# Optimization experiments

Measured on AMD Instinct MI355X. Metric: run time of the kernel, lower is better.

## Reference

```python
import jax, jax.numpy as jnp
import numpy as np

DIM = 8
EPS = 1e-6
TRIL = DIM * (DIM + 1) // 2  # 36


def _build_L(params):
    # params: [N, TRIL] -> lower-triangular L: [N, DIM, DIM] with diag clamped >= 1e-4
    rows, cols = jnp.tril_indices(DIM)
    L = jnp.zeros((params.shape[0], DIM, DIM), params.dtype)
    L = L.at[:, rows, cols].set(params)
    idx = jnp.arange(DIM)
    d = jnp.clip(L[:, idx, idx], 0.0001)
    return L.at[:, idx, idx].set(d)


def _compute_density(L):
    # L: [N, DIM, DIM] -> PSD trace-1 density matrices [N, DIM, DIM]
    I = jnp.eye(DIM, dtype=L.dtype)
    rho = jnp.einsum('nij,nkj->nik', L, L) + EPS * I
    w = jnp.linalg.eigvalsh(rho)                      # [N, DIM]
    corr = jnp.maximum(-w.min(axis=-1), 0.0) + 1e-6   # shift to PSD
    rho = rho + corr[:, None, None] * I
    tr = jnp.trace(rho, axis1=1, axis2=2)
    return rho / (tr[:, None, None] + EPS)


def _matrix_sqrt(x):
    U, S, Vh = jnp.linalg.svd(x, full_matrices=False)
    sqrt_S = jnp.sqrt(S + EPS)
    return (U * sqrt_S[..., None, :]) @ Vh


def _quantum_fidelity(rho, sigma):
    sqrt_rho = _matrix_sqrt(rho)
    product = sqrt_rho @ sigma @ sqrt_rho
    S = jnp.linalg.svd(product, compute_uv=False)
    f = jnp.sum(jnp.sqrt(S + EPS), axis=-1)
    return jnp.clip(f, 0.0, 1.0)


def setup_inputs() -> dict:
    key = jax.random.key(0)
    k1, k2, k3 = jax.random.split(key, 3)
    B, S, V = 16384, 10, 100000
    contexts = jax.random.randint(k1, (B, S), 0, V)
    targets = jax.random.randint(k2, (B,), 0, V)
    # embedding table, init roughly like the torch module (uniform + diag ramp)
    emb_weight = jax.random.uniform(k3, (V, TRIL), jnp.float32, -0.1, 0.1)
    diag_idx = np.array([i * (i + 1) // 2 + i for i in range(DIM)])
    diag_vals = jnp.linspace(0.1, 1.0, DIM, dtype=jnp.float32)
    emb_weight = emb_weight.at[:, diag_idx].set(jnp.broadcast_to(diag_vals, (V, DIM)))
    return {"contexts": contexts, "targets": targets, "emb_weight": emb_weight}


def reference(contexts, targets, emb_weight):
    B, S = contexts.shape
    # context density matrices
    ctx_params = jnp.take(emb_weight, contexts.reshape(-1), axis=0)   # [B*S, TRIL]
    rho_ctx = _compute_density(_build_L(ctx_params)).reshape(B, S, DIM, DIM)
    mask = (contexts != 0).astype(rho_ctx.dtype)[:, :, None, None]
    context_rho = (rho_ctx * mask).sum(axis=1) / mask.sum(axis=1)     # [B, DIM, DIM]
    # target density matrices
    tgt_params = jnp.take(emb_weight, targets, axis=0)                # [B, TRIL]
    rho_tgt = _compute_density(_build_L(tgt_params))                  # [B, DIM, DIM]
    f = _quantum_fidelity(context_rho, rho_tgt)                       # [B]
    return -jnp.log(jnp.clip(f, 1e-8))
```

## Files before the change

### kernel.cpp

```cpp
#include <hip/hip_runtime.h>
#include <math.h>

#define NB   16384
#define SEQ  10
#define DIM  8
#define TRIL 36

__device__ __forceinline__ constexpr int tri(int r, int c) { return r * (r + 1) / 2 + c; }

template <int CTRL>
__device__ __forceinline__ float fperm(float v) {
    return __int_as_float(__builtin_amdgcn_mov_dpp(__float_as_int(v), CTRL, 0xf, 0xf, true));
}
template <int CTRL>
__device__ __forceinline__ double dperm(double v) {
    long long u = __double_as_longlong(v);
    int lo = (int)(u & 0xffffffffLL);
    int hi = (int)(u >> 32);
    lo = __builtin_amdgcn_mov_dpp(lo, CTRL, 0xf, 0xf, true);
    hi = __builtin_amdgcn_mov_dpp(hi, CTRL, 0xf, 0xf, true);
    return __longlong_as_double(((long long)hi << 32) | (long long)(unsigned)lo);
}

__device__ __forceinline__ double fast_rsqrt(double x) {
    double r = __builtin_amdgcn_rsq(x);
    r = r * (1.5 - 0.5 * x * r * r);
    r = r * (1.5 - 0.5 * x * r * r);
    return r;
}
__device__ __forceinline__ double fast_rcp(double x) {
    double r = __builtin_amdgcn_rcp(x);
    r = r * (2.0 - x * r);
    r = r * (2.0 - x * r);
    return r;
}
__device__ __forceinline__ double fast_sqrt(double x) { return x * fast_rsqrt(x); }

template <bool ACCUM>
__device__ __forceinline__ void add_density(const float* __restrict__ p, double (&dst)[TRIL]) {
    float Lf[TRIL];
    const float4* p4 = (const float4*)p;
    #pragma unroll
    for (int i = 0; i < 9; ++i) {
        float4 v = p4[i];
        Lf[4*i+0] = v.x; Lf[4*i+1] = v.y; Lf[4*i+2] = v.z; Lf[4*i+3] = v.w;
    }
    #pragma unroll
    for (int d = 0; d < DIM; ++d) Lf[tri(d, d)] = fmaxf(Lf[tri(d, d)], 1.0e-4f);

    double tr = 1.6e-5;
    #pragma unroll
    for (int i = 0; i < TRIL; ++i) { double v = (double)Lf[i]; tr += v * v; }
    double inv = fast_rcp(tr + 1.0e-6);

    #pragma unroll
    for (int i = 0; i < DIM; ++i) {
        #pragma unroll
        for (int j = 0; j <= i; ++j) {
            double sum = (i == j) ? 2.0e-6 : 0.0;
            #pragma unroll
            for (int k = 0; k <= j; ++k) sum += (double)Lf[tri(i, k)] * (double)Lf[tri(j, k)];
            if (ACCUM) dst[tri(i, j)] += sum * inv;
            else       dst[tri(i, j)]  = sum * inv;
        }
    }
}

__device__ __forceinline__ void chol36(double (&M)[TRIL]) {
    #pragma unroll
    for (int j = 0; j < DIM; ++j) {
        double d = M[tri(j, j)];
        #pragma unroll
        for (int k = 0; k < j; ++k) d -= M[tri(j, k)] * M[tri(j, k)];
        d = fmax(d, 1.0e-30);
        double invd = fast_rsqrt(d);
        M[tri(j, j)] = d * invd;
        #pragma unroll
        for (int i = j + 1; i < DIM; ++i) {
            double v = M[tri(i, j)];
            #pragma unroll
            for (int k = 0; k < j; ++k) v -= M[tri(i, k)] * M[tri(j, k)];
            M[tri(i, j)] = v * invd;
        }
    }
}

__global__ void __launch_bounds__(64)
qcbow_kernel(const int* __restrict__ contexts,
             const int* __restrict__ targets,
             const float* __restrict__ emb,
             float* __restrict__ out)
{
    const int tid = blockIdx.x * 64 + threadIdx.x;
    const int b = tid >> 2;
    const int g = threadIdx.x & 3;

    double A[TRIL];
    #pragma unroll
    for (int i = 0; i < TRIL; ++i) A[i] = 0.0;
    float cntf = 0.0f;
    for (int s = g; s < SEQ; s += 4) {
        int tok = contexts[b * SEQ + s];
        if (tok != 0) {
            add_density<true>(emb + (size_t)tok * TRIL, A);
            cntf += 1.0f;
        }
    }

    double W[TRIL];
    add_density<false>(emb + (size_t)targets[b] * TRIL, W);

    #pragma unroll
    for (int i = 0; i < TRIL; ++i) A[i] += dperm<0xB1>(A[i]);
    cntf += fperm<0xB1>(cntf);
    #pragma unroll
    for (int i = 0; i < TRIL; ++i) A[i] += dperm<0x4E>(A[i]);
    cntf += fperm<0x4E>(cntf);

    chol36(W);

    double invc = fast_rcp((double)cntf);
    #pragma unroll
    for (int i = 0; i < TRIL; ++i) A[i] *= invc;
    #pragma unroll
    for (int d = 0; d < DIM; ++d) A[tri(d, d)] += 1.0e-6;
    chol36(A);

    double wa[DIM], wb[DIM];
#define PICKW(JA, JB)                                                              \
    {                                                                              \
        _Pragma("unroll")                                                          \
        for (int k = 0; k < DIM; ++k) wa[k] = (k >= (JA)) ? W[tri(k, (JA))] : 0.0; \
        _Pragma("unroll")                                                          \
        for (int k = 0; k < DIM; ++k) wb[k] = (k >= (JB)) ? W[tri(k, (JB))] : 0.0; \
    }
    switch (g) {
        case 0: PICKW(0, 1); break;
        case 1: PICKW(2, 3); break;
        case 2: PICKW(4, 5); break;
        default: PICKW(6, 7); break;
    }
#undef PICKW

    float a[DIM], bb[DIM];
    #pragma unroll
    for (int i = 0; i < DIM; ++i) {
        double sa = 0.0, sb = 0.0;
        #pragma unroll
        for (int k = i; k < DIM; ++k) {
            double lk = A[tri(k, i)];
            sa += lk * wa[k];
            sb += lk * wb[k];
        }
        a[i] = (float)sa; bb[i] = (float)sb;
    }

    for (int sweep = 0; sweep < 8; ++sweep) {
        bool conv = true;
        #pragma unroll
        for (int r = 0; r < 7; ++r) {
            float x = 0.0f, y = 0.0f, z = 0.0f;
            #pragma unroll
            for (int k = 0; k < DIM; ++k) {
                x = fmaf(a[k], a[k], x);
                y = fmaf(bb[k], bb[k], y);
                z = fmaf(a[k], bb[k], z);
            }
            float z2 = z * z;
            float d  = x - y;
            if (z2 > 1.0e-12f * x * y && z2 > 1.0e-12f * d * d) conv = false;
            if (z2 > 1.0e-16f * x * y) {
                float tau = -d * (0.5f * __builtin_amdgcn_rcpf(z));
                float t = __builtin_amdgcn_rcpf(fabsf(tau) + sqrtf(fmaf(tau, tau, 1.0f)));
                t = (tau >= 0.0f) ? t : -t;
                float c = __builtin_amdgcn_rsqf(fmaf(t, t, 1.0f));
                float s = t * c;
                #pragma unroll
                for (int k = 0; k < DIM; ++k) {
                    float na = c * a[k] - s * bb[k];
                    float nb = s * a[k] + c * bb[k];
                    a[k] = na; bb[k] = nb;
                }
            }
            #pragma unroll
            for (int k = 0; k < DIM; ++k) {
                float olda = a[k];
                float sa = (g == 0) ? bb[k] : a[k];
                float ta = fperm<0x93>(sa);
                float tb = fperm<0x39>(bb[k]);
                a[k]  = (g == 0) ? olda : ta;
                bb[k] = (g == 3) ? olda : tb;
            }
        }
        if (sweep >= 2 && __all(conv)) break;
    }

    double xn = 0.0, yn = 0.0;
    #pragma unroll
    for (int k = 0; k < DIM; ++k) {
        xn += (double)a[k] * (double)a[k];
        yn += (double)bb[k] * (double)bb[k];
    }
    double fp = fast_sqrt(xn + 1.0e-6) + fast_sqrt(yn + 1.0e-6);
    fp += dperm<0xB1>(fp);
    fp += dperm<0x4E>(fp);
    if (g == 0) {
        double f = fmin(fp, 1.0);
        f = fmax(f, 1.0e-8);
        out[b] = (float)(-log(f));
    }
}

extern "C" void kernel_launch(void* const* d_in, const int* in_sizes, int n_in,
                              void* d_out, int out_size, void* d_ws, size_t ws_size,
                              hipStream_t stream) {
    const int*   contexts = (const int*)d_in[0];
    const int*   targets  = (const int*)d_in[1];
    const float* emb      = (const float*)d_in[2];
    float*       out      = (float*)d_out;

    qcbow_kernel<<<dim3(NB * 4 / 64), dim3(64), 0, stream>>>(contexts, targets, emb, out);
}
```

Measured before the change: 85.81 us.

## Spread each batch item over eight lanes with one-column-per-lane Jacobi

Each batch element is now handled by 8 lanes instead of 4. Every lane loads its context and target rows up front, and the two Cholesky factorizations (context and target) run in parallel on separate half-groups. The result is exchanged with ds_swizzle. The one-sided Jacobi SVD is reorganised so each lane owns one column, using a round-robin partner exchange through DPP and swizzle. This cuts per-thread serial work and register pressure, at the cost of more cross-lane shuffles and duplicated density computation for the target on some lanes.

New measurement: 86.99 us. About the same (+1.4%).

```diff
diff --git a/kernel.cpp b/kernel.cpp
--- a/kernel.cpp
+++ b/kernel.cpp
@@ -16,9 +16,20 @@
 __device__ __forceinline__ double dperm(double v) {
     long long u = __double_as_longlong(v);
     int lo = (int)(u & 0xffffffffLL);
-    int hi = (int)(u >> 32);
+    int hi = (int)(((unsigned long long)u) >> 32);
     lo = __builtin_amdgcn_mov_dpp(lo, CTRL, 0xf, 0xf, true);
     hi = __builtin_amdgcn_mov_dpp(hi, CTRL, 0xf, 0xf, true);
+    return __longlong_as_double(((long long)hi << 32) | (long long)(unsigned)lo);
+}
+__device__ __forceinline__ float fswz4(float v) {
+    return __int_as_float(__builtin_amdgcn_ds_swizzle(__float_as_int(v), 0x101F));
+}
+__device__ __forceinline__ double dswz4(double v) {
+    long long u = __double_as_longlong(v);
+    int lo = (int)(u & 0xffffffffLL);
+    int hi = (int)(((unsigned long long)u) >> 32);
+    lo = __builtin_amdgcn_ds_swizzle(lo, 0x101F);
+    hi = __builtin_amdgcn_ds_swizzle(hi, 0x101F);
     return __longlong_as_double(((long long)hi << 32) | (long long)(unsigned)lo);
 }
 
@@ -36,23 +47,23 @@
 }
 __device__ __forceinline__ double fast_sqrt(double x) { return x * fast_rsqrt(x); }
 
+__device__ __forceinline__ void load_row(const float* __restrict__ emb, int tok, float (&F)[TRIL]) {
+    const float4* q = (const float4*)(emb + (size_t)tok * TRIL);
+    #pragma unroll
+    for (int i = 0; i < 9; ++i) {
+        float4 v = q[i];
+        F[4*i+0] = v.x; F[4*i+1] = v.y; F[4*i+2] = v.z; F[4*i+3] = v.w;
+    }
+}
+
 template <bool ACCUM>
-__device__ __forceinline__ void add_density(const float* __restrict__ p, double (&dst)[TRIL]) {
-    float Lf[TRIL];
-    const float4* p4 = (const float4*)p;
-    #pragma unroll
-    for (int i = 0; i < 9; ++i) {
-        float4 v = p4[i];
-        Lf[4*i+0] = v.x; Lf[4*i+1] = v.y; Lf[4*i+2] = v.z; Lf[4*i+3] = v.w;
-    }
+__device__ __forceinline__ void density_from(float (&Lf)[TRIL], double (&dst)[TRIL]) {
     #pragma unroll
     for (int d = 0; d < DIM; ++d) Lf[tri(d, d)] = fmaxf(Lf[tri(d, d)], 1.0e-4f);
-
     double tr = 1.6e-5;
     #pragma unroll
     for (int i = 0; i < TRIL; ++i) { double v = (double)Lf[i]; tr += v * v; }
     double inv = fast_rcp(tr + 1.0e-6);
-
     #pragma unroll
     for (int i = 0; i < DIM; ++i) {
         #pragma unroll
@@ -85,30 +96,72 @@
     }
 }
 
-__global__ void __launch_bounds__(64)
+template <int M>
+__device__ __forceinline__ float jrecv(float v) {
+    if constexpr (M == 1) return fperm<0xB1>(v);
+    else if constexpr (M == 2) return fperm<0x4E>(v);
+    else if constexpr (M == 3) return fperm<0x1B>(v);
+    else return __int_as_float(__builtin_amdgcn_ds_swizzle(__float_as_int(v), (M << 10) | 0x1F));
+}
+template <int M>
+__device__ __forceinline__ void jround(float (&o)[DIM], bool& conv) {
+    float r[DIM];
+    #pragma unroll
+    for (int k = 0; k < DIM; ++k) r[k] = jrecv<M>(o[k]);
+    float xo = 0.0f, xr = 0.0f, z = 0.0f;
+    #pragma unroll
+    for (int k = 0; k < DIM; ++k) {
+        xo = fmaf(o[k], o[k], xo);
+        xr = fmaf(r[k], r[k], xr);
+        z  = fmaf(o[k], r[k], z);
+    }
+    float z2 = z * z;
+    float d  = xr - xo;
+    if (z2 > 1.0e-12f * xo * xr && z2 > 1.0e-12f * d * d) conv = false;
+    if (z2 > 1.0e-16f * xo * xr) {
+        float tau = d * (0.5f * __builtin_amdgcn_rcpf(z));
+        float t = __builtin_amdgcn_rcpf(fabsf(tau) + sqrtf(fmaf(tau, tau, 1.0f)));
+        t = (tau >= 0.0f) ? t : -t;
+        float c = __builtin_amdgcn_rsqf(fmaf(t, t, 1.0f));
+        float s = t * c;
+        #pragma unroll
+        for (int k = 0; k < DIM; ++k) o[k] = fmaf(c, o[k], -s * r[k]);
+    }
+}
+
+__global__ void __launch_bounds__(256, 2)
 qcbow_kernel(const int* __restrict__ contexts,
              const int* __restrict__ targets,
              const float* __restrict__ emb,
              float* __restrict__ out)
 {
-    const int tid = blockIdx.x * 64 + threadIdx.x;
-    const int b = tid >> 2;
-    const int g = threadIdx.x & 3;
+    const int tid = blockIdx.x * 256 + threadIdx.x;
+    const int b = tid >> 3;
+    const int h = threadIdx.x & 7;
+
+    const int base = b * SEQ;
+    int tok1 = contexts[base + h];
+    int tok2 = 0;
+    if (h < 2)  tok2 = contexts[base + 8 + h];
+    if (h >= 4) tok2 = targets[b];
+
+    float F1[TRIL], F2[TRIL];
+    load_row(emb, tok1, F1);
+    load_row(emb, tok2, F2);
 
     double A[TRIL];
     #pragma unroll
     for (int i = 0; i < TRIL; ++i) A[i] = 0.0;
     float cntf = 0.0f;
-    for (int s = g; s < SEQ; s += 4) {
-        int tok = contexts[b * SEQ + s];
-        if (tok != 0) {
-            add_density<true>(emb + (size_t)tok * TRIL, A);
-            cntf += 1.0f;
-        }
-    }
-
-    double W[TRIL];
-    add_density<false>(emb + (size_t)targets[b] * TRIL, W);
+
+    if (tok1 != 0) { density_from<true>(F1, A); cntf = 1.0f; }
+    double T[TRIL];
+    density_from<false>(F2, T);
+    if (h < 2 && tok2 != 0) {
+        #pragma unroll
+        for (int i = 0; i < TRIL; ++i) A[i] += T[i];
+        cntf += 1.0f;
+    }
 
     #pragma unroll
     for (int i = 0; i < TRIL; ++i) A[i] += dperm<0xB1>(A[i]);
@@ -116,95 +169,76 @@
     #pragma unroll
     for (int i = 0; i < TRIL; ++i) A[i] += dperm<0x4E>(A[i]);
     cntf += fperm<0x4E>(cntf);
-
-    chol36(W);
+    #pragma unroll
+    for (int i = 0; i < TRIL; ++i) A[i] += dswz4(A[i]);
+    cntf += fswz4(cntf);
 
     double invc = fast_rcp((double)cntf);
     #pragma unroll
     for (int i = 0; i < TRIL; ++i) A[i] *= invc;
     #pragma unroll
     for (int d = 0; d < DIM; ++d) A[tri(d, d)] += 1.0e-6;
-    chol36(A);
-
-    double wa[DIM], wb[DIM];
-#define PICKW(JA, JB)                                                              \
-    {                                                                              \
-        _Pragma("unroll")                                                          \
-        for (int k = 0; k < DIM; ++k) wa[k] = (k >= (JA)) ? W[tri(k, (JA))] : 0.0; \
-        _Pragma("unroll")                                                          \
-        for (int k = 0; k < DIM; ++k) wb[k] = (k >= (JB)) ? W[tri(k, (JB))] : 0.0; \
-    }
-    switch (g) {
-        case 0: PICKW(0, 1); break;
-        case 1: PICKW(2, 3); break;
-        case 2: PICKW(4, 5); break;
-        default: PICKW(6, 7); break;
-    }
-#undef PICKW
-
-    float a[DIM], bb[DIM];
+
+    const bool q0 = (h < 4);
+    double M[TRIL];
+    #pragma unroll
+    for (int i = 0; i < TRIL; ++i) M[i] = q0 ? A[i] : T[i];
+    chol36(M);
+
+    double Rm[TRIL];
+    #pragma unroll
+    for (int i = 0; i < TRIL; ++i) Rm[i] = dswz4(M[i]);
+
+    double Lw_[TRIL];
+    #pragma unroll
+    for (int i = 0; i < TRIL; ++i) Lw_[i] = q0 ? Rm[i] : M[i];
+    const bool h1 = (h & 1), h2 = (h & 2), h4 = (h & 4);
+    double w[DIM];
+    #pragma unroll
+    for (int k = 0; k < DIM; ++k) {
+        #define E(J) ((k >= (J)) ? Lw_[tri((k >= (J)) ? k : (J), (J))] : 0.0)
+        double m0 = h1 ? E(1) : E(0);
+        double m1 = h1 ? E(3) : E(2);
+        double m2 = h1 ? E(5) : E(4);
+        double m3 = h1 ? E(7) : E(6);
+        #undef E
+        double n0 = h2 ? m1 : m0;
+        double n1 = h2 ? m3 : m2;
+        w[k] = h4 ? n1 : n0;
+    }
+
+    float col[DIM];
     #pragma unroll
     for (int i = 0; i < DIM; ++i) {
-        double sa = 0.0, sb = 0.0;
+        double s = 0.0;
         #pragma unroll
         for (int k = i; k < DIM; ++k) {
-            double lk = A[tri(k, i)];
-            sa += lk * wa[k];
-            sb += lk * wb[k];
+            double lc = q0 ? M[tri(k, i)] : Rm[tri(k, i)];
+            s += lc * w[k];
         }
-        a[i] = (float)sa; bb[i] = (float)sb;
+        col[i] = (float)s;
     }
 
     for (int sweep = 0; sweep < 8; ++sweep) {
         bool conv = true;
-        #pragma unroll
-        for (int r = 0; r < 7; ++r) {
-            float x = 0.0f, y = 0.0f, z = 0.0f;
-            #pragma unroll
-            for (int k = 0; k < DIM; ++k) {
-                x = fmaf(a[k], a[k], x);
-                y = fmaf(bb[k], bb[k], y);
-                z = fmaf(a[k], bb[k], z);
-            }
-            float z2 = z * z;
-            float d  = x - y;
-            if (z2 > 1.0e-12f * x * y && z2 > 1.0e-12f * d * d) conv = false;
-            if (z2 > 1.0e-16f * x * y) {
-                float tau = -d * (0.5f * __builtin_amdgcn_rcpf(z));
-                float t = __builtin_amdgcn_rcpf(fabsf(tau) + sqrtf(fmaf(tau, tau, 1.0f)));
-                t = (tau >= 0.0f) ? t : -t;
-                float c = __builtin_amdgcn_rsqf(fmaf(t, t, 1.0f));
-                float s = t * c;
-                #pragma unroll
-                for (int k = 0; k < DIM; ++k) {
-                    float na = c * a[k] - s * bb[k];
-                    float nb = s * a[k] + c * bb[k];
-                    a[k] = na; bb[k] = nb;
-                }
-            }
-            #pragma unroll
-            for (int k = 0; k < DIM; ++k) {
-                float olda = a[k];
-                float sa = (g == 0) ? bb[k] : a[k];
-                float ta = fperm<0x93>(sa);
-                float tb = fperm<0x39>(bb[k]);
-                a[k]  = (g == 0) ? olda : ta;
-                bb[k] = (g == 3) ? olda : tb;
-            }
-        }
+        jround<1>(col, conv);
+        jround<2>(col, conv);
+        jround<3>(col, conv);
+        jround<4>(col, conv);
+        jround<5>(col, conv);
+        jround<6>(col, conv);
+        jround<7>(col, conv);
         if (sweep >= 2 && __all(conv)) break;
     }
 
-    double xn = 0.0, yn = 0.0;
-    #pragma unroll
-    for (int k = 0; k < DIM; ++k) {
-        xn += (double)a[k] * (double)a[k];
-        yn += (double)bb[k] * (double)bb[k];
-    }
-    double fp = fast_sqrt(xn + 1.0e-6) + fast_sqrt(yn + 1.0e-6);
+    double xn = 0.0;
+    #pragma unroll
+    for (int k = 0; k < DIM; ++k) xn += (double)col[k] * (double)col[k];
+    double fp = fast_sqrt(xn + 1.0e-6);
     fp += dperm<0xB1>(fp);
     fp += dperm<0x4E>(fp);
-    if (g == 0) {
+    fp += dswz4(fp);
+    if (h == 0) {
         double f = fmin(fp, 1.0);
         f = fmax(f, 1.0e-8);
         out[b] = (float)(-log(f));
@@ -219,5 +253,5 @@
     const float* emb      = (const float*)d_in[2];
     float*       out      = (float*)d_out;
 
-    qcbow_kernel<<<dim3(NB * 4 / 64), dim3(64), 0, stream>>>(contexts, targets, emb, out);
-}
+    qcbow_kernel<<<dim3(NB * 8 / 256), dim3(256), 0, stream>>>(contexts, targets, emb, out);
+}
```
